# Performance work log

Measured on AMD Instinct MI355X. Metric: run time of the kernel, lower is better.

The kernel has to match this reference:

```python
import jax, jax.numpy as jnp
import numpy as np

B, S, D = 2, 4096, 768
H = 12
HD = D // H  # 64


def setup_inputs() -> dict:
    key = jax.random.key(0)
    ks = jax.random.split(key, 5)
    scale = 1.0 / np.sqrt(D)
    x = jax.random.normal(ks[0], (B, S, D), dtype=jnp.float32)
    Wq = jax.random.normal(ks[1], (D, D), dtype=jnp.float32) * scale
    Wk = jax.random.normal(ks[2], (D, D), dtype=jnp.float32) * scale
    Wv = jax.random.normal(ks[3], (D, D), dtype=jnp.float32) * scale
    Wo = jax.random.normal(ks[4], (D, D), dtype=jnp.float32) * scale
    zb = jnp.zeros((D,), dtype=jnp.float32)
    return {"x": x, "Wq": Wq, "bq": zb, "Wk": Wk, "bk": zb, "Wv": Wv, "bv": zb, "Wo": Wo, "bo": zb}


def reference(x, Wq, bq, Wk, bk, Wv, bv, Wo, bo):
    b, s, d = x.shape
    # projections: nn.Linear computes x @ W^T + b; here W is stored as [in, out]-style [D, D]
    def proj(W, bias):
        y = jnp.einsum('bsd,ed->bse', x, W) + bias  # matches torch Linear (weight [out,in])
        return y.reshape(b, s, H, HD).transpose(0, 2, 1, 3)  # [B,H,S,HD]
    q = proj(Wq, bq)
    k = proj(Wk, bk)
    v = proj(Wv, bv)
    att = jnp.einsum('bhqd,bhkd->bhqk', q, k) / np.sqrt(HD).astype(np.float32)
    causal = jnp.tril(jnp.ones((s, s), dtype=bool))
    att = jnp.where(causal, att, -jnp.inf)
    att = jax.nn.softmax(att, axis=-1)  # dropout p=0 (eval)
    y = jnp.einsum('bhqk,bhkd->bhqd', att, v)
    y = y.transpose(0, 2, 1, 3).reshape(b, s, d)
    return jnp.einsum('bsd,ed->bse', y, Wo) + bo
```

## Files before the change

kernel.cpp:

```cpp
#include <hip/hip_runtime.h>
#include <hip/hip_bf16.h>

typedef __bf16 bf16;
typedef __attribute__((ext_vector_type(8))) __bf16 bf16x8;
typedef __attribute__((ext_vector_type(4))) __bf16 bf16x4;
typedef __attribute__((ext_vector_type(4))) float f32x4;
typedef __attribute__((ext_vector_type(16))) float f32x16;

#if __has_builtin(__builtin_amdgcn_permlane32_swap)
#define HAVE_PLSWAP 1
typedef __attribute__((ext_vector_type(2))) unsigned uint2v;
#endif

#define MFMA16(a, b, c) __builtin_amdgcn_mfma_f32_16x16x32_bf16((a), (b), (c), 0, 0, 0)
#define MFMA32(a, b, c) __builtin_amdgcn_mfma_f32_32x32x16_bf16((a), (b), (c), 0, 0, 0)

__device__ __forceinline__ void gload_lds16(const bf16* g, bf16* l) {
  __builtin_amdgcn_global_load_lds(
      (const __attribute__((address_space(1))) void*)g,
      (__attribute__((address_space(3))) void*)l, 16, 0, 0);
}

__device__ __forceinline__ unsigned pkbf(float a, float b) {
  union { unsigned u; bf16 h[2]; } w;
  w.h[0] = (bf16)a; w.h[1] = (bf16)b;
  return w.u;
}

__device__ __forceinline__ float mx3(float a, float b, float c) {
  return fmaxf(fmaxf(a, b), c);
}

__global__ void cvt_all(const float* __restrict__ x,
                        const float* __restrict__ wq, const float* __restrict__ wk,
                        const float* __restrict__ wv, const float* __restrict__ wo,
                        bf16* __restrict__ xb, bf16* __restrict__ Wb) {
  constexpr int NX4 = 6291456 / 4;
  constexpr int NW4 = 589824 / 4;
  constexpr int TOT = NX4 + 4 * NW4;
  int stride = gridDim.x * blockDim.x;
  for (int i = blockIdx.x * blockDim.x + threadIdx.x; i < TOT; i += stride) {
    const float4* src;
    bf16x4* dst;
    if (i < NX4) {
      src = reinterpret_cast<const float4*>(x) + i;
      dst = reinterpret_cast<bf16x4*>(xb) + i;
    } else {
      int j = i - NX4;
      int w = j / NW4, r = j - w * NW4;
      const float* sp = (w == 0) ? wq : (w == 1) ? wk : (w == 2) ? wv : wo;
      src = reinterpret_cast<const float4*>(sp) + r;
      dst = reinterpret_cast<bf16x4*>(Wb) + j;
    }
    float4 v = *src;
    bf16x4 o = {(bf16)v.x, (bf16)v.y, (bf16)v.z, (bf16)v.w};
    *dst = o;
  }
}

template <bool OUT_BF16>
__global__ __launch_bounds__(256) void gemm_bt(
    const bf16* __restrict__ A, const bf16* __restrict__ W,
    const float* __restrict__ b0, const float* __restrict__ b1, const float* __restrict__ b2,
    float* __restrict__ Cf, bf16* __restrict__ Cb,
    int M, int N, int K) {
  const int z = blockIdx.z;
  const bf16* Wz = W + (size_t)z * N * K;
  const float* bias = (z == 0) ? b0 : (z == 1 ? b1 : b2);

  __shared__ alignas(16) bf16 As[128 * 64];
  __shared__ alignas(16) bf16 Bs[128 * 64];

  const int tid = threadIdx.x;
  const int wave = tid >> 6, lane = tid & 63;
  const int lr = lane & 15, lg = lane >> 4;
  const int wr = wave >> 1, wc = wave & 1;
  const int m0 = blockIdx.y * 128, n0 = blockIdx.x * 128;

  f32x4 acc[4][4] = {};

  for (int k0 = 0; k0 < K; k0 += 64) {
    __syncthreads();
#pragma unroll
    for (int j = 0; j < 4; ++j) {
      int cb = j * 256 + wave * 64;
      int c = cb + lane;
      int row = c >> 3, x = c & 7;
      int xs = x ^ (row & 7);
      gload_lds16(&A[(size_t)(m0 + row) * K + k0 + xs * 8], &As[cb * 8]);
      gload_lds16(&Wz[(size_t)(n0 + row) * K + k0 + xs * 8], &Bs[cb * 8]);
    }
    __syncthreads();
#pragma unroll
    for (int kk = 0; kk < 2; ++kk) {
      bf16x8 af[4], bfr[4];
#pragma unroll
      for (int m = 0; m < 4; ++m) {
        int row = wr * 64 + m * 16 + lr;
        int ch = (kk * 4 + lg) ^ (row & 7);
        af[m] = *reinterpret_cast<const bf16x8*>(&As[row * 64 + ch * 8]);
      }
#pragma unroll
      for (int n = 0; n < 4; ++n) {
        int row = wc * 64 + n * 16 + lr;
        int ch = (kk * 4 + lg) ^ (row & 7);
        bfr[n] = *reinterpret_cast<const bf16x8*>(&Bs[row * 64 + ch * 8]);
      }
      __builtin_amdgcn_s_setprio(1);
#pragma unroll
      for (int m = 0; m < 4; ++m)
#pragma unroll
        for (int n = 0; n < 4; ++n)
          acc[m][n] = MFMA16(af[m], bfr[n], acc[m][n]);
      __builtin_amdgcn_s_setprio(0);
    }
  }

#pragma unroll
  for (int m = 0; m < 4; ++m) {
#pragma unroll
    for (int n = 0; n < 4; ++n) {
#pragma unroll
      for (int i = 0; i < 4; ++i) {
        int row = m0 + wr * 64 + m * 16 + lg * 4 + i;
        int col = n0 + wc * 64 + n * 16 + lr;
        float v = acc[m][n][i] + bias[col];
        if constexpr (OUT_BF16)
          (Cb + (size_t)z * M * N)[(size_t)row * N + col] = (bf16)v;
        else
          Cf[(size_t)row * N + col] = v;
      }
    }
  }
}

__global__ __launch_bounds__(128, 2) void attn32(
    const bf16* __restrict__ Q, const bf16* __restrict__ K,
    const bf16* __restrict__ V, bf16* __restrict__ Y) {
  constexpr int S = 4096, D = 768;
  const int lin = blockIdx.x;
  const int xcd = lin & 7, idx = lin >> 3;
  const int pair = xcd * 3 + (idx >> 6);
  const int qs = 63 - (idx & 63);
  const int h = pair % 12, bb = pair / 12;

  const int tid = threadIdx.x, wave = tid >> 6, lane = tid & 63;
  const int ln = lane & 31, hi = lane >> 5;
  const int q0s = qs * 64;
  const int qw0 = q0s + wave * 32;
  const int qrow = qw0 + ln;

  __shared__ alignas(16) bf16 Ks[2][64 * 64];
  __shared__ alignas(16) bf16 Vt[2][64 * 64];

  const size_t head = (size_t)bb * S * D + (size_t)h * 64;
  const float SC2 = 0.125f * 1.44269504089f;

  union U32x4 { unsigned u[4]; bf16x8 v; };
  U32x4 onesU;
  onesU.u[0] = onesU.u[1] = onesU.u[2] = onesU.u[3] = 0x3F803F80u;
  const bf16x8 onesf = onesU.v;

  bf16x8 qf[4];
  {
    const bf16* qp = Q + head + (size_t)qrow * D;
#pragma unroll
    for (int c = 0; c < 4; ++c) {
      bf16x8 t = *reinterpret_cast<const bf16x8*>(qp + c * 16 + hi * 8);
#pragma unroll
      for (int e = 0; e < 8; ++e) t[e] = (bf16)((float)t[e] * SC2);
      qf[c] = t;
    }
  }

  int fOff[4];
#pragma unroll
  for (int i = 0; i < 4; ++i)
    fOff[i] = ln * 64 + ((((2 * i + hi) ^ ln) & 7) * 8);

  const bf16* gk[4];
  int ldsK[4];
#pragma unroll
  for (int j = 0; j < 4; ++j) {
    int c = j * 128 + tid;
    int r = c >> 3, ch = c & 7;
    gk[j] = K + head + (size_t)r * D + ((ch ^ (r & 7)) & 7) * 8;
    ldsK[j] = (j * 128 + wave * 64) * 8;
  }

  const int k0v = (tid & 15) * 4, d0 = (tid >> 4) * 8;
  const bf16* gv[4];
#pragma unroll
  for (int m = 0; m < 4; ++m) gv[m] = V + head + (size_t)(k0v + m) * D + d0;
  int wOff[8];
#pragma unroll
  for (int e = 0; e < 8; ++e)
    wOff[e] = (d0 + e) * 64 + ((((k0v >> 3) ^ e) & 7) * 8) + (k0v & 7);

  f32x16 accO0 = {}, accO1 = {}, accL = {};
  float mrun = 8.0f;

  auto stageK = [&](int buf) {
#pragma unroll
    for (int j = 0; j < 4; ++j) {
      gload_lds16(gk[j], &Ks[buf][ldsK[j]]);
      gk[j] += 64 * D;
    }
  };
  auto loadV = [&](bf16x8* vv) {
#pragma unroll
    for (int m = 0; m < 4; ++m) {
      vv[m] = *reinterpret_cast<const bf16x8*>(gv[m]);
      gv[m] += 64 * D;
    }
  };
  auto writeV = [&](const bf16x8* vv, int buf) {
#pragma unroll
    for (int e = 0; e < 8; ++e) {
      bf16x4 pw = {vv[0][e], vv[1][e], vv[2][e], vv[3][e]};
      *reinterpret_cast<bf16x4*>(&Vt[buf][wOff[e]]) = pw;
    }
  };

  const int nt = qs + 1;

  {
    bf16x8 v0[4];
    loadV(v0);
    stageK(0);
    writeV(v0, 0);
  }
  __syncthreads();

  int cur = 0;
  for (int t = 0; t < nt; ++t) {
    const int kv0 = t * 64;
    const bool more = (t + 1 < nt);
    bf16x8 vnext[4];
    if (more) {
      loadV(vnext);
      stageK(cur ^ 1);
    }

    f32x16 s0 = {}, s1 = {};
    __builtin_amdgcn_s_setprio(1);
#pragma unroll
    for (int c = 0; c < 4; ++c) {
      bf16x8 kf0 = *reinterpret_cast<const bf16x8*>(&Ks[cur][fOff[c]]);
      bf16x8 kf1 = *reinterpret_cast<const bf16x8*>(&Ks[cur][fOff[c] + 2048]);
      s0 = MFMA32(kf0, qf[c], s0);
      s1 = MFMA32(kf1, qf[c], s1);
    }
    __builtin_amdgcn_s_setprio(0);

    if (kv0 + 63 > qw0) {
#pragma unroll
      for (int r = 0; r < 16; ++r) {
        int kl = (r & 3) + 8 * (r >> 2) + 4 * hi;
        if (kv0 + kl > qrow) s0[r] = -1e30f;
        if (kv0 + 32 + kl > qrow) s1[r] = -1e30f;
      }
    }

    float p[32];
#pragma unroll
    for (int r = 0; r < 16; ++r) {
      p[r] = __builtin_amdgcn_exp2f(s0[r] - mrun);
      p[16 + r] = __builtin_amdgcn_exp2f(s1[r] - mrun);
    }

    float t0 = mx3(s0[0], s0[1], s0[2]);
    float t1 = mx3(s0[3], s0[4], s0[5]);
    float t2 = mx3(s0[6], s0[7], s0[8]);
    float t3 = mx3(s0[9], s0[10], s0[11]);
    float t4 = mx3(s0[12], s0[13], s0[14]);
    float t5 = mx3(s0[15], s1[0], s1[1]);
    float t6 = mx3(s1[2], s1[3], s1[4]);
    float t7 = mx3(s1[5], s1[6], s1[7]);
    float t8 = mx3(s1[8], s1[9], s1[10]);
    float t9 = mx3(s1[11], s1[12], s1[13]);
    float ta = fmaxf(s1[14], s1[15]);
    float u0 = mx3(t0, t1, t2);
    float u1 = mx3(t3, t4, t5);
    float u2 = mx3(t6, t7, t8);
    float u3 = fmaxf(t9, ta);
    float pm = fmaxf(mx3(u0, u1, u2), u3);

    if (!__all(pm - mrun <= 8.0f)) {
      float pm2 = fmaxf(pm, __shfl_xor(pm, 32));
      float mnew = fmaxf(mrun, pm2);
      float alpha = __builtin_amdgcn_exp2f(mrun - mnew);
      mrun = mnew;
      accL[0] *= alpha;
#pragma unroll
      for (int r = 0; r < 16; ++r) {
        accO0[r] *= alpha; accO1[r] *= alpha;
        p[r] *= alpha; p[16 + r] *= alpha;
      }
    }

    __builtin_amdgcn_s_setprio(1);
#pragma unroll
    for (int kg = 0; kg < 2; ++kg) {
      const float* pv = &p[kg * 16];
      unsigned w0 = pkbf(pv[0], pv[1]), w1 = pkbf(pv[2], pv[3]);
      unsigned w2 = pkbf(pv[4], pv[5]), w3 = pkbf(pv[6], pv[7]);
      unsigned w4 = pkbf(pv[8], pv[9]), w5 = pkbf(pv[10], pv[11]);
      unsigned w6 = pkbf(pv[12], pv[13]), w7 = pkbf(pv[14], pv[15]);
      union { unsigned u[4]; bf16x8 v; } fe, fo;
#if HAVE_PLSWAP
      uint2v r02 = __builtin_amdgcn_permlane32_swap(w0, w2, false, false);
      uint2v r13 = __builtin_amdgcn_permlane32_swap(w1, w3, false, false);
      uint2v r46 = __builtin_amdgcn_permlane32_swap(w4, w6, false, false);
      uint2v r57 = __builtin_amdgcn_permlane32_swap(w5, w7, false, false);
      fe.u[0] = r02.x; fe.u[1] = r13.x; fe.u[2] = r02.y; fe.u[3] = r13.y;
      fo.u[0] = r46.x; fo.u[1] = r57.x; fo.u[2] = r46.y; fo.u[3] = r57.y;
#else
      unsigned X0 = hi ? w0 : w2, X1 = hi ? w1 : w3;
      unsigned X2 = hi ? w4 : w6, X3 = hi ? w5 : w7;
      unsigned Y0 = __shfl_xor((int)X0, 32), Y1 = __shfl_xor((int)X1, 32);
      unsigned Y2 = __shfl_xor((int)X2, 32), Y3 = __shfl_xor((int)X3, 32);
      fe.u[0] = hi ? Y0 : w0; fe.u[1] = hi ? Y1 : w1;
      fe.u[2] = hi ? w2 : Y0; fe.u[3] = hi ? w3 : Y1;
      fo.u[0] = hi ? Y2 : w4; fo.u[1] = hi ? Y3 : w5;
      fo.u[2] = hi ? w6 : Y2; fo.u[3] = hi ? w7 : Y3;
#endif
#pragma unroll
      for (int half = 0; half < 2; ++half) {
        int kc = 2 * kg + half;
        bf16x8 pf = half ? fo.v : fe.v;
        bf16x8 vf0 = *reinterpret_cast<const bf16x8*>(&Vt[cur][fOff[kc]]);
        bf16x8 vf1 = *reinterpret_cast<const bf16x8*>(&Vt[cur][fOff[kc] + 2048]);
        accO0 = MFMA32(vf0, pf, accO0);
        accO1 = MFMA32(vf1, pf, accO1);
        accL = MFMA32(onesf, pf, accL);
      }
    }
    __builtin_amdgcn_s_setprio(0);

    if (more) {
      writeV(vnext, cur ^ 1);
      __syncthreads();
      cur ^= 1;
    }
  }

  float inv = 1.f / accL[0];
  bf16* yp = Y + head + (size_t)qrow * D;
#pragma unroll
  for (int g = 0; g < 4; ++g) {
    bf16x4 o0, o1;
#pragma unroll
    for (int i = 0; i < 4; ++i) {
      o0[i] = (bf16)(accO0[g * 4 + i] * inv);
      o1[i] = (bf16)(accO1[g * 4 + i] * inv);
    }
    *reinterpret_cast<bf16x4*>(yp + 8 * g + 4 * hi) = o0;
    *reinterpret_cast<bf16x4*>(yp + 32 + 8 * g + 4 * hi) = o1;
  }
}

extern "C" void kernel_launch(void* const* d_in, const int* in_sizes, int n_in,
                              void* d_out, int out_size, void* d_ws, size_t ws_size,
                              hipStream_t stream) {
  const float* x  = (const float*)d_in[0];
  const float* Wq = (const float*)d_in[1];
  const float* bq = (const float*)d_in[2];
  const float* Wk = (const float*)d_in[3];
  const float* bk = (const float*)d_in[4];
  const float* Wv = (const float*)d_in[5];
  const float* bv = (const float*)d_in[6];
  const float* Wo = (const float*)d_in[7];
  const float* bo = (const float*)d_in[8];
  float* out = (float*)d_out;

  constexpr int Bx = 2, S = 4096, Dd = 768;
  constexpr int M = Bx * S;
  constexpr size_t XB = (size_t)M * Dd;
  constexpr size_t WB = (size_t)Dd * Dd;

  char* ws = (char*)d_ws;
  bf16* xb = (bf16*)ws;
  bf16* Wb = (bf16*)(ws + 2 * XB);
  bf16* Qb = (bf16*)(ws + 2 * XB + 8 * WB);
  bf16* Kb = Qb + XB;
  bf16* Vb = Kb + XB;
  bf16* Yb = Vb + XB;

  cvt_all<<<2048, 256, 0, stream>>>(x, Wq, Wk, Wv, Wo, xb, Wb);

  gemm_bt<true><<<dim3(6, 64, 3), 256, 0, stream>>>(
      xb, Wb, bq, bk, bv, nullptr, Qb, M, Dd, Dd);

  attn32<<<dim3(1536), 128, 0, stream>>>(Qb, Kb, Vb, Yb);

  gemm_bt<false><<<dim3(6, 64, 1), 256, 0, stream>>>(
      Yb, Wb + 3 * WB, bo, bo, bo, out, nullptr, M, Dd, Dd);
}
```

Before: 196.6 us.

## Single-buffer K/V LDS tiles via register staging to raise attention occupancy

Replaces the double-buffered K/V shared-memory tiles with single buffers and stages K through registers instead of direct global-to-LDS loads. The next tile's K and V are prefetched into registers during compute and written to LDS between two barriers. Launch bounds go from 2 to 4 blocks per SM to exploit the smaller LDS footprint. This halves LDS use but adds an extra barrier per tile and more register pressure, which may limit the intended occupancy gain.

```diff
diff --git a/kernel.cpp b/kernel.cpp
--- a/kernel.cpp
+++ b/kernel.cpp
@@ -134,7 +134,7 @@
   }
 }
 
-__global__ __launch_bounds__(128, 2) void attn32(
+__global__ __launch_bounds__(128, 4) void attn32(
     const bf16* __restrict__ Q, const bf16* __restrict__ K,
     const bf16* __restrict__ V, bf16* __restrict__ Y) {
   constexpr int S = 4096, D = 768;
@@ -150,8 +150,8 @@
   const int qw0 = q0s + wave * 32;
   const int qrow = qw0 + ln;
 
-  __shared__ alignas(16) bf16 Ks[2][64 * 64];
-  __shared__ alignas(16) bf16 Vt[2][64 * 64];
+  __shared__ alignas(16) bf16 Ks[64 * 64];
+  __shared__ alignas(16) bf16 Vt[64 * 64];
 
   const size_t head = (size_t)bb * S * D + (size_t)h * 64;
   const float SC2 = 0.125f * 1.44269504089f;
@@ -179,13 +179,13 @@
     fOff[i] = ln * 64 + ((((2 * i + hi) ^ ln) & 7) * 8);
 
   const bf16* gk[4];
-  int ldsK[4];
+  int wKOff[4];
 #pragma unroll
   for (int j = 0; j < 4; ++j) {
     int c = j * 128 + tid;
     int r = c >> 3, ch = c & 7;
-    gk[j] = K + head + (size_t)r * D + ((ch ^ (r & 7)) & 7) * 8;
-    ldsK[j] = (j * 128 + wave * 64) * 8;
+    gk[j] = K + head + (size_t)r * D + ch * 8;
+    wKOff[j] = r * 64 + ((ch ^ (r & 7)) & 7) * 8;
   }
 
   const int k0v = (tid & 15) * 4, d0 = (tid >> 4) * 8;
@@ -200,12 +200,17 @@
   f32x16 accO0 = {}, accO1 = {}, accL = {};
   float mrun = 8.0f;
 
-  auto stageK = [&](int buf) {
+  auto loadK = [&](bf16x8* kk) {
 #pragma unroll
     for (int j = 0; j < 4; ++j) {
-      gload_lds16(gk[j], &Ks[buf][ldsK[j]]);
+      kk[j] = *reinterpret_cast<const bf16x8*>(gk[j]);
       gk[j] += 64 * D;
     }
+  };
+  auto writeK = [&](const bf16x8* kk) {
+#pragma unroll
+    for (int j = 0; j < 4; ++j)
+      *reinterpret_cast<bf16x8*>(&Ks[wKOff[j]]) = kk[j];
   };
   auto loadV = [&](bf16x8* vv) {
 #pragma unroll
@@ -214,40 +219,40 @@
       gv[m] += 64 * D;
     }
   };
-  auto writeV = [&](const bf16x8* vv, int buf) {
+  auto writeV = [&](const bf16x8* vv) {
 #pragma unroll
     for (int e = 0; e < 8; ++e) {
       bf16x4 pw = {vv[0][e], vv[1][e], vv[2][e], vv[3][e]};
-      *reinterpret_cast<bf16x4*>(&Vt[buf][wOff[e]]) = pw;
+      *reinterpret_cast<bf16x4*>(&Vt[wOff[e]]) = pw;
     }
   };
 
   const int nt = qs + 1;
 
   {
-    bf16x8 v0[4];
+    bf16x8 k0[4], v0[4];
+    loadK(k0);
     loadV(v0);
-    stageK(0);
-    writeV(v0, 0);
+    writeK(k0);
+    writeV(v0);
   }
   __syncthreads();
 
-  int cur = 0;
   for (int t = 0; t < nt; ++t) {
     const int kv0 = t * 64;
     const bool more = (t + 1 < nt);
-    bf16x8 vnext[4];
+    bf16x8 knext[4], vnext[4];
     if (more) {
+      loadK(knext);
       loadV(vnext);
-      stageK(cur ^ 1);
     }
 
     f32x16 s0 = {}, s1 = {};
     __builtin_amdgcn_s_setprio(1);
 #pragma unroll
     for (int c = 0; c < 4; ++c) {
-      bf16x8 kf0 = *reinterpret_cast<const bf16x8*>(&Ks[cur][fOff[c]]);
-      bf16x8 kf1 = *reinterpret_cast<const bf16x8*>(&Ks[cur][fOff[c] + 2048]);
+      bf16x8 kf0 = *reinterpret_cast<const bf16x8*>(&Ks[fOff[c]]);
+      bf16x8 kf1 = *reinterpret_cast<const bf16x8*>(&Ks[fOff[c] + 2048]);
       s0 = MFMA32(kf0, qf[c], s0);
       s1 = MFMA32(kf1, qf[c], s1);
     }
@@ -329,8 +334,8 @@
       for (int half = 0; half < 2; ++half) {
         int kc = 2 * kg + half;
         bf16x8 pf = half ? fo.v : fe.v;
-        bf16x8 vf0 = *reinterpret_cast<const bf16x8*>(&Vt[cur][fOff[kc]]);
-        bf16x8 vf1 = *reinterpret_cast<const bf16x8*>(&Vt[cur][fOff[kc] + 2048]);
+        bf16x8 vf0 = *reinterpret_cast<const bf16x8*>(&Vt[fOff[kc]]);
+        bf16x8 vf1 = *reinterpret_cast<const bf16x8*>(&Vt[fOff[kc] + 2048]);
         accO0 = MFMA32(vf0, pf, accO0);
         accO1 = MFMA32(vf1, pf, accO1);
         accL = MFMA32(onesf, pf, accL);
@@ -339,9 +344,10 @@
     __builtin_amdgcn_s_setprio(0);
 
     if (more) {
-      writeV(vnext, cur ^ 1);
       __syncthreads();
-      cur ^= 1;
+      writeK(knext);
+      writeV(vnext);
+      __syncthreads();
     }
   }
 
```

Measured after the change: 702.0 us. 3.57x slower.

## Single-buffer V tile in LDS and interleave causal block ordering

Applied to the files above, without the earlier changes.

The V transpose buffer in shared memory drops from double to single buffering, which saves 8 KB of LDS per block and may allow more resident blocks. To keep this safe, a barrier is added before V is written each iteration, at the cost of an extra sync per tile. The query-block order within each head pair also changes from strictly descending to a mixed order (the first half descending from the top, the second half ascending from zero). This rebalances the causal workload across the dispatch order.

```diff
diff --git a/kernel.cpp b/kernel.cpp
--- a/kernel.cpp
+++ b/kernel.cpp
@@ -141,7 +141,8 @@
   const int lin = blockIdx.x;
   const int xcd = lin & 7, idx = lin >> 3;
   const int pair = xcd * 3 + (idx >> 6);
-  const int qs = 63 - (idx & 63);
+  const int j = idx & 63;
+  const int qs = (j < 32) ? (63 - j) : (j - 32);
   const int h = pair % 12, bb = pair / 12;
 
   const int tid = threadIdx.x, wave = tid >> 6, lane = tid & 63;
@@ -151,7 +152,7 @@
   const int qrow = qw0 + ln;
 
   __shared__ alignas(16) bf16 Ks[2][64 * 64];
-  __shared__ alignas(16) bf16 Vt[2][64 * 64];
+  __shared__ alignas(16) bf16 Vt[64 * 64];
 
   const size_t head = (size_t)bb * S * D + (size_t)h * 64;
   const float SC2 = 0.125f * 1.44269504089f;
@@ -181,11 +182,11 @@
   const bf16* gk[4];
   int ldsK[4];
 #pragma unroll
-  for (int j = 0; j < 4; ++j) {
-    int c = j * 128 + tid;
+  for (int j2 = 0; j2 < 4; ++j2) {
+    int c = j2 * 128 + tid;
     int r = c >> 3, ch = c & 7;
-    gk[j] = K + head + (size_t)r * D + ((ch ^ (r & 7)) & 7) * 8;
-    ldsK[j] = (j * 128 + wave * 64) * 8;
+    gk[j2] = K + head + (size_t)r * D + ((ch ^ (r & 7)) & 7) * 8;
+    ldsK[j2] = (j2 * 128 + wave * 64) * 8;
   }
 
   const int k0v = (tid & 15) * 4, d0 = (tid >> 4) * 8;
@@ -202,9 +203,9 @@
 
   auto stageK = [&](int buf) {
 #pragma unroll
-    for (int j = 0; j < 4; ++j) {
-      gload_lds16(gk[j], &Ks[buf][ldsK[j]]);
-      gk[j] += 64 * D;
+    for (int j2 = 0; j2 < 4; ++j2) {
+      gload_lds16(gk[j2], &Ks[buf][ldsK[j2]]);
+      gk[j2] += 64 * D;
     }
   };
   auto loadV = [&](bf16x8* vv) {
@@ -214,11 +215,11 @@
       gv[m] += 64 * D;
     }
   };
-  auto writeV = [&](const bf16x8* vv, int buf) {
+  auto writeV = [&](const bf16x8* vv) {
 #pragma unroll
     for (int e = 0; e < 8; ++e) {
       bf16x4 pw = {vv[0][e], vv[1][e], vv[2][e], vv[3][e]};
-      *reinterpret_cast<bf16x4*>(&Vt[buf][wOff[e]]) = pw;
+      *reinterpret_cast<bf16x4*>(&Vt[wOff[e]]) = pw;
     }
   };
 
@@ -228,7 +229,7 @@
     bf16x8 v0[4];
     loadV(v0);
     stageK(0);
-    writeV(v0, 0);
+    writeV(v0);
   }
   __syncthreads();
 
@@ -329,8 +330,8 @@
       for (int half = 0; half < 2; ++half) {
         int kc = 2 * kg + half;
         bf16x8 pf = half ? fo.v : fe.v;
-        bf16x8 vf0 = *reinterpret_cast<const bf16x8*>(&Vt[cur][fOff[kc]]);
-        bf16x8 vf1 = *reinterpret_cast<const bf16x8*>(&Vt[cur][fOff[kc] + 2048]);
+        bf16x8 vf0 = *reinterpret_cast<const bf16x8*>(&Vt[fOff[kc]]);
+        bf16x8 vf1 = *reinterpret_cast<const bf16x8*>(&Vt[fOff[kc] + 2048]);
         accO0 = MFMA32(vf0, pf, accO0);
         accO1 = MFMA32(vf1, pf, accO1);
         accL = MFMA32(onesf, pf, accL);
@@ -339,7 +340,8 @@
     __builtin_amdgcn_s_setprio(0);
 
     if (more) {
-      writeV(vnext, cur ^ 1);
+      __syncthreads();
+      writeV(vnext);
       __syncthreads();
       cur ^= 1;
     }
```

After: 201.8 us. 1.03x slower.
